# Performance work log

Measured on AMD Instinct MI355X. Metric: run time of the kernel, lower is better.

## Reference

```python
import jax, jax.numpy as jnp
import numpy as np

D_MODEL = 1024
D_MEM = 256


def setup_inputs() -> dict:
    key = jax.random.key(0)
    ks = jax.random.split(key, 12)
    b, s = 4, 2048
    sc_d = 1.0 / np.sqrt(D_MODEL)
    sc_m = 1.0 / np.sqrt(D_MEM)
    return {
        "x": jax.random.normal(ks[0], (b, s, D_MODEL), dtype=jnp.float32),
        "state": jnp.zeros((b, D_MEM, D_MEM), dtype=jnp.float32),
        "Wk": jax.random.normal(ks[1], (D_MODEL, D_MEM), dtype=jnp.float32) * sc_d,
        "bk": jnp.zeros((D_MEM,), dtype=jnp.float32),
        "Wv": jax.random.normal(ks[2], (D_MODEL, D_MEM), dtype=jnp.float32) * sc_d,
        "bv": jnp.zeros((D_MEM,), dtype=jnp.float32),
        "Wq": jax.random.normal(ks[3], (D_MODEL, D_MEM), dtype=jnp.float32) * sc_d,
        "bq": jnp.zeros((D_MEM,), dtype=jnp.float32),
        "Wo": jax.random.normal(ks[4], (D_MEM, D_MODEL), dtype=jnp.float32) * sc_m,
        "bo": jnp.zeros((D_MODEL,), dtype=jnp.float32),
        "Wg": jax.random.normal(ks[5], (D_MODEL, 1), dtype=jnp.float32) * sc_d,
        "bg": jnp.zeros((1,), dtype=jnp.float32),
        "decay": jnp.float32(0.95),
    }


def reference(x, state, Wk, bk, Wv, bv, Wq, bq, Wo, bo, Wg, bg, decay):
    # projections: [b, s, d_mem]
    k = x @ Wk + bk
    v = x @ Wv + bv
    q = x @ Wq + bq
    surprise = jax.nn.sigmoid(x @ Wg + bg)  # [b, s, 1]

    # time-major for scan: [s, b, ...]
    kT = jnp.swapaxes(k, 0, 1)
    vT = jnp.swapaxes(v, 0, 1)
    qT = jnp.swapaxes(q, 0, 1)
    sT = jnp.swapaxes(surprise, 0, 1)  # [s, b, 1]

    def step(S, inp):
        k_t, v_t, q_t, s_t = inp  # [b,dm],[b,dm],[b,dm],[b,1]
        # read: q_t (row) @ S  -> [b, dm]
        mem_out = jnp.einsum('bd,bde->be', q_t, S)
        # write: decayed rank-1 outer-product update, gated by surprise
        assoc = jnp.einsum('bd,be->bde', v_t, k_t)  # v k^T
        S_new = decay * S + s_t[:, :, None] * assoc
        return S_new, mem_out

    final_state, outs = jax.lax.scan(step, state, (kT, vT, qT, sT))
    outputs = jnp.swapaxes(outs, 0, 1)  # [b, s, dm]
    y = outputs @ Wo + bo  # [b, s, d_model]
    return y, final_state
```

## Files before the change

### kernel.cpp

```cpp
#include <hip/hip_runtime.h>
#include <math.h>


using bf16x8 = __attribute__((ext_vector_type(8))) short;
using f32x4  = __attribute__((ext_vector_type(4))) float;
using u16x4  = __attribute__((ext_vector_type(4))) unsigned short;
using u16x8  = __attribute__((ext_vector_type(8))) unsigned short;

__device__ inline unsigned short f2bf(float f) {
  unsigned int u = __float_as_uint(f);
  u = (u + 0x7FFF + ((u >> 16) & 1)) >> 16;
  return (unsigned short)u;
}
__device__ inline float bf2f(unsigned short u) {
  return __uint_as_float(((unsigned int)u) << 16);
}

#define GLD_LDS(gsrc, ldst) \
  __builtin_amdgcn_global_load_lds( \
      (const __attribute__((address_space(1))) unsigned int*)(gsrc), \
      (__attribute__((address_space(3))) unsigned int*)(ldst), 16, 0, 0)

struct MP {
  const unsigned short* A; long long a_bs; int lda;
  const unsigned short* B; long long b_bs; int ldb;
  int K, grid_n;
  unsigned short* Cb; long long c_bs; int ldc;
};

__global__ __launch_bounds__(256)
void gemm_ut(MP p) {
  __shared__ unsigned short As[128 * 64];
  __shared__ unsigned short Bs[128 * 64];
  const int tid = threadIdx.x;
  const int bid = blockIdx.x;
  const int bn = bid % p.grid_n, bm = bid / p.grid_n;
  const int m0 = bm * 128, n0 = bn * 128;
  const long long z = blockIdx.z;
  const int lane = tid & 63, wv = tid >> 6;
  const int wr = wv >> 1, wc = wv & 1;
  const int srow = tid >> 3, scol = (tid & 7) * 8;

  f32x4 acc[4][4] = {};

  const unsigned short* Abase = p.A + z * p.a_bs + (long long)m0 * p.lda;
  const unsigned short* Bbase = p.B + z * p.b_bs + (long long)n0 * p.ldb;

  for (int k0 = 0; k0 < p.K; k0 += 64) {
    if (k0) __syncthreads();
#pragma unroll
    for (int i = 0; i < 4; i++) {
      int row = i * 32 + srow;
      GLD_LDS(Abase + (long long)row * p.lda + k0 + scol, &As[row * 64 + scol]);
    }
#pragma unroll
    for (int i = 0; i < 4; i++) {
      int row = i * 32 + srow;
      GLD_LDS(Bbase + (long long)row * p.ldb + k0 + scol, &Bs[row * 64 + scol]);
    }
    __syncthreads();
#pragma unroll
    for (int kk = 0; kk < 2; kk++) {
      bf16x8 af[4], bfr[4];
      const int kb = kk * 32 + 8 * (lane >> 4);
#pragma unroll
      for (int m = 0; m < 4; m++)
        af[m] = *(const bf16x8*)&As[(wr * 64 + m * 16 + (lane & 15)) * 64 + kb];
#pragma unroll
      for (int n = 0; n < 4; n++)
        bfr[n] = *(const bf16x8*)&Bs[(wc * 64 + n * 16 + (lane & 15)) * 64 + kb];
#pragma unroll
      for (int m = 0; m < 4; m++)
#pragma unroll
        for (int n = 0; n < 4; n++)
          acc[m][n] = __builtin_amdgcn_mfma_f32_16x16x32_bf16(af[m], bfr[n], acc[m][n], 0, 0, 0);
    }
  }

  const int crow0 = m0 + wr * 64, ccol0 = n0 + wc * 64;
#pragma unroll
  for (int m = 0; m < 4; m++) {
#pragma unroll
    for (int n = 0; n < 4; n++) {
      int col = ccol0 + n * 16 + (lane & 15);
#pragma unroll
      for (int q = 0; q < 4; q++) {
        int row = crow0 + m * 16 + (lane >> 4) * 4 + q;
        p.Cb[z * p.c_bs + (long long)row * p.ldc + col] = f2bf(acc[m][n][q]);
      }
    }
  }
}

__global__ __launch_bounds__(256)
void proj_kernel(const unsigned short* __restrict__ x16, const unsigned short* __restrict__ w16,
                 const float* __restrict__ bk, const float* __restrict__ bv,
                 const float* __restrict__ bq, const float* __restrict__ gate,
                 const float* __restrict__ decay_ptr,
                 unsigned short* __restrict__ o_v, unsigned short* __restrict__ o_qd,
                 unsigned short* __restrict__ o_kT, unsigned short* __restrict__ o_vTw) {
  __shared__ unsigned short As[64 * 64];
  __shared__ unsigned short Bs[128 * 64];
  __shared__ float warr[64];
  const int tid = threadIdx.x;
  const int bid = (blockIdx.x & 7) * (gridDim.x >> 3) + (blockIdx.x >> 3);
  const int bn = bid % 6, bm = bid / 6;
  const int m0 = bm * 64, n0 = bn * 128;
  const int lane = tid & 63, wv = tid >> 6;
  const int srow = tid >> 3, scol = (tid & 7) * 8;

  f32x4 acc[4][2] = {};
  const unsigned short* Abase = x16 + (long long)m0 * 1024;
  const unsigned short* Bbase = w16 + (long long)n0 * 1024;

  for (int k0 = 0; k0 < 1024; k0 += 64) {
    if (k0) __syncthreads();
#pragma unroll
    for (int i = 0; i < 2; i++) {
      int row = i * 32 + srow;
      GLD_LDS(Abase + (long long)row * 1024 + k0 + scol, &As[row * 64 + scol]);
    }
#pragma unroll
    for (int i = 0; i < 4; i++) {
      int row = i * 32 + srow;
      GLD_LDS(Bbase + (long long)row * 1024 + k0 + scol, &Bs[row * 64 + scol]);
    }
    __syncthreads();
#pragma unroll
    for (int kk = 0; kk < 2; kk++) {
      const int kb = kk * 32 + 8 * (lane >> 4);
      bf16x8 af[4], bfr[2];
#pragma unroll
      for (int m = 0; m < 4; m++)
        af[m] = *(const bf16x8*)&As[(m * 16 + (lane & 15)) * 64 + kb];
#pragma unroll
      for (int n = 0; n < 2; n++)
        bfr[n] = *(const bf16x8*)&Bs[(wv * 32 + n * 16 + (lane & 15)) * 64 + kb];
#pragma unroll
      for (int m = 0; m < 4; m++)
#pragma unroll
        for (int n = 0; n < 2; n++)
          acc[m][n] = __builtin_amdgcn_mfma_f32_16x16x32_bf16(af[m], bfr[n], acc[m][n], 0, 0, 0);
    }
  }

  const float log2d = log2f(decay_ptr[0]);
  const int sel = bn >> 1;
  const int half = bn & 1;
  const int z = bm >> 1, jbase = (bm & 1) * 64;

  if (sel < 2) {
    __syncthreads();
    if (sel == 1 && tid < 64)
      warr[tid] = gate[z * 128 + jbase + tid] * exp2f((float)(127 - (jbase + tid)) * log2d);
  }

#pragma unroll
  for (int m = 0; m < 4; m++) {
#pragma unroll
    for (int n = 0; n < 2; n++) {
      int cl = wv * 32 + n * 16 + (lane & 15);
      int r0 = m * 16 + (lane >> 4) * 4;
      float bias = (sel == 0) ? bk[half * 128 + cl]
                 : (sel == 1) ? bv[half * 128 + cl]
                 : bq[half * 128 + cl];
      if (sel < 2) {
        u16x4 pk;
#pragma unroll
        for (int q = 0; q < 4; q++) {
          float v = acc[m][n][q] + bias;
          pk[q] = f2bf(v);
          if (sel == 1)
            o_v[((long long)m0 + r0 + q) * 256 + half * 128 + cl] = pk[q];
        }
        int byteoff = (cl * 128 + r0 * 2) ^ ((cl & 7) << 4);
        *(u16x4*)((char*)Bs + byteoff) = pk;
      } else {
#pragma unroll
        for (int q = 0; q < 4; q++) {
          long long row = m0 + r0 + q;
          float v = acc[m][n][q] + bias;
          o_qd[row * 256 + half * 128 + cl] =
              f2bf(v * exp2f((float)(jbase + r0 + q) * log2d));
        }
      }
    }
  }

  if (sel < 2) {
    __syncthreads();
    unsigned short* dst = (sel == 0 ? o_kT : o_vTw) + (long long)z * 32768;
#pragma unroll
    for (int pp = 0; pp < 4; pp++) {
      int idx = pp * 256 + tid;
      int c = idx >> 3;
      int j0 = (idx & 7) * 8;
      u16x8 o = *(const u16x8*)((char*)Bs + ((c * 128 + j0 * 2) ^ ((c & 7) << 4)));
      if (sel == 1) {
#pragma unroll
        for (int t = 0; t < 8; t++) o[t] = f2bf(bf2f(o[t]) * warr[j0 + t]);
      }
      *(u16x8*)&dst[(long long)(half * 128 + c) * 128 + jbase + j0] = o;
    }
  }
}

__global__ __launch_bounds__(256)
void y64_kernel(const unsigned short* __restrict__ mo16, const unsigned short* __restrict__ wot16,
                const float* __restrict__ bo, float* __restrict__ out_y) {
  __shared__ unsigned short As[64 * 64];
  __shared__ unsigned short Bs[128 * 64];
  const int tid = threadIdx.x;
  const int bid = (blockIdx.x & 7) * (gridDim.x >> 3) + (blockIdx.x >> 3);
  const int bn = bid & 7, bm = bid >> 3;
  const int m0 = bm * 64, n0 = bn * 128;
  const int lane = tid & 63, wv = tid >> 6;
  const int srow = tid >> 3, scol = (tid & 7) * 8;

  f32x4 acc[4][2] = {};
  const unsigned short* Abase = mo16 + (long long)m0 * 256;
  const unsigned short* Bbase = wot16 + (long long)n0 * 256;

  for (int k0 = 0; k0 < 256; k0 += 64) {
    if (k0) __syncthreads();
#pragma unroll
    for (int i = 0; i < 2; i++) {
      int row = i * 32 + srow;
      GLD_LDS(Abase + (long long)row * 256 + k0 + scol, &As[row * 64 + scol]);
    }
#pragma unroll
    for (int i = 0; i < 4; i++) {
      int row = i * 32 + srow;
      GLD_LDS(Bbase + (long long)row * 256 + k0 + scol, &Bs[row * 64 + scol]);
    }
    __syncthreads();
#pragma unroll
    for (int kk = 0; kk < 2; kk++) {
      const int kb = kk * 32 + 8 * (lane >> 4);
      bf16x8 af[4], bfr[2];
#pragma unroll
      for (int m = 0; m < 4; m++)
        af[m] = *(const bf16x8*)&As[(m * 16 + (lane & 15)) * 64 + kb];
#pragma unroll
      for (int n = 0; n < 2; n++)
        bfr[n] = *(const bf16x8*)&Bs[(wv * 32 + n * 16 + (lane & 15)) * 64 + kb];
#pragma unroll
      for (int m = 0; m < 4; m++)
#pragma unroll
        for (int n = 0; n < 2; n++)
          acc[m][n] = __builtin_amdgcn_mfma_f32_16x16x32_bf16(af[m], bfr[n], acc[m][n], 0, 0, 0);
    }
  }

#pragma unroll
  for (int m = 0; m < 4; m++) {
#pragma unroll
    for (int n = 0; n < 2; n++) {
      int col = n0 + wv * 32 + n * 16 + (lane & 15);
      float b = bo[col];
#pragma unroll
      for (int q = 0; q < 4; q++) {
        int row = m0 + m * 16 + (lane >> 4) * 4 + q;
        out_y[(long long)row * 1024 + col] = acc[m][n][q] + b;
      }
    }
  }
}

__global__ __launch_bounds__(512)
void chunk_attn(const unsigned short* __restrict__ qd16, const unsigned short* __restrict__ v16,
                const unsigned short* __restrict__ kT16, const unsigned short* __restrict__ T16,
                unsigned short* __restrict__ mo16, const float* __restrict__ gbuf,
                const float* __restrict__ decay_ptr) {
  __shared__ unsigned short As[64 * 64];
  __shared__ unsigned short Bs[2 * 128 * 64];
  __shared__ unsigned short Al[64 * 128];
  const int tid = threadIdx.x, lane = tid & 63, wv = tid >> 6;
  const int wr = wv >> 2, wc = wv & 3;
  const int nh = blockIdx.x, rh = blockIdx.y, z = blockIdx.z;
  const int roff = rh * 64;
  const int srow = tid >> 3, scol = (tid & 7) * 8;
  const float log2d = log2f(decay_ptr[0]);

  const unsigned short* qz = qd16 + (long long)z * 32768 + (long long)roff * 256;
  const unsigned short* vz = v16 + (long long)z * 32768;
  const unsigned short* Tz = T16 + (long long)z * 65536 + (long long)nh * 128 * 256;
  const unsigned short* kz = kT16 + (long long)z * 32768 + (long long)nh * 128 * 128;

  f32x4 acc1[2][2] = {};
  f32x4 acc2[2][2] = {};

  for (int k0 = 0; k0 < 256; k0 += 64) {
    if (k0) __syncthreads();
    GLD_LDS(qz + (long long)srow * 256 + k0 + scol, &As[srow * 64 + scol]);
#pragma unroll
    for (int i = 0; i < 2; i++) {
      int row = i * 64 + srow;
      GLD_LDS(vz + (long long)row * 256 + k0 + scol, &Bs[row * 64 + scol]);
      GLD_LDS(Tz + (long long)row * 256 + k0 + scol, &Bs[8192 + row * 64 + scol]);
    }
    __syncthreads();
#pragma unroll
    for (int kk = 0; kk < 2; kk++) {
      const int kb = kk * 32 + 8 * (lane >> 4);
      bf16x8 af[2], bv[2], bt[2];
#pragma unroll
      for (int m = 0; m < 2; m++)
        af[m] = *(const bf16x8*)&As[(wr * 32 + m * 16 + (lane & 15)) * 64 + kb];
#pragma unroll
      for (int n = 0; n < 2; n++) {
        bv[n] = *(const bf16x8*)&Bs[(wc * 32 + n * 16 + (lane & 15)) * 64 + kb];
        bt[n] = *(const bf16x8*)&Bs[8192 + (wc * 32 + n * 16 + (lane & 15)) * 64 + kb];
      }
#pragma unroll
      for (int m = 0; m < 2; m++)
#pragma unroll
        for (int n = 0; n < 2; n++) {
          acc1[m][n] = __builtin_amdgcn_mfma_f32_16x16x32_bf16(af[m], bv[n], acc1[m][n], 0, 0, 0);
          acc2[m][n] = __builtin_amdgcn_mfma_f32_16x16x32_bf16(af[m], bt[n], acc2[m][n], 0, 0, 0);
        }
    }
  }

#pragma unroll
  for (int n = 0; n < 2; n++) {
    int col = wc * 32 + n * 16 + (lane & 15);
    float gsc = gbuf[z * 128 + col] * exp2f(-(float)(col + 1) * log2d);
#pragma unroll
    for (int m = 0; m < 2; m++) {
#pragma unroll
      for (int q = 0; q < 4; q++) {
        int r = wr * 32 + m * 16 + (lane >> 4) * 4 + q;
        float v = (col < roff + r) ? acc1[m][n][q] * gsc : 0.f;
        int byteoff = (r * 256 + col * 2) ^ ((r & 7) << 4);
        *(unsigned short*)((char*)Al + byteoff) = f2bf(v);
      }
    }
  }
  __syncthreads();

  for (int k0 = 0; k0 < 128; k0 += 64) {
    if (k0) __syncthreads();
#pragma unroll
    for (int i = 0; i < 2; i++) {
      int row = i * 64 + srow;
      GLD_LDS(kz + (long long)row * 128 + k0 + scol, &Bs[row * 64 + scol]);
    }
    __syncthreads();
#pragma unroll
    for (int kk = 0; kk < 2; kk++) {
      const int kbb = k0 + kk * 32 + 8 * (lane >> 4);
      bf16x8 af[2], bk_[2];
#pragma unroll
      for (int m = 0; m < 2; m++) {
        int r = wr * 32 + m * 16 + (lane & 15);
        af[m] = *(const bf16x8*)((char*)Al + ((r * 256 + kbb * 2) ^ ((r & 7) << 4)));
      }
#pragma unroll
      for (int n = 0; n < 2; n++)
        bk_[n] = *(const bf16x8*)&Bs[(wc * 32 + n * 16 + (lane & 15)) * 64 + kk * 32 + 8 * (lane >> 4)];
#pragma unroll
      for (int m = 0; m < 2; m++)
#pragma unroll
        for (int n = 0; n < 2; n++)
          acc2[m][n] = __builtin_amdgcn_mfma_f32_16x16x32_bf16(af[m], bk_[n], acc2[m][n], 0, 0, 0);
    }
  }

#pragma unroll
  for (int m = 0; m < 2; m++) {
#pragma unroll
    for (int n = 0; n < 2; n++) {
      int col = nh * 128 + wc * 32 + n * 16 + (lane & 15);
#pragma unroll
      for (int q = 0; q < 4; q++) {
        int row = roff + wr * 32 + m * 16 + (lane >> 4) * 4 + q;
        mo16[((long long)z * 128 + row) * 256 + col] = f2bf(acc2[m][n][q]);
      }
    }
  }
}

__global__ __launch_bounds__(256)
void prep_kernel(const float* __restrict__ x, const float* __restrict__ Wg,
                 const float* __restrict__ bg, unsigned short* __restrict__ x16,
                 float* __restrict__ g,
                 const float* __restrict__ Wk, const float* __restrict__ Wv,
                 const float* __restrict__ Wq, unsigned short* __restrict__ w16,
                 const float* __restrict__ Wo, unsigned short* __restrict__ wot16) {
  __shared__ float tile[64][65];
  const int bx = blockIdx.x;
  const int tid = threadIdx.x;
  if (bx < 2048) {
    const int wave = tid >> 6, lane = tid & 63;
    const long long row = (long long)bx * 4 + wave;
    const float* xr = x + row * 1024 + lane * 16;
    const float* wr = Wg + lane * 16;
    float s = 0.f;
    u16x8 o0, o1;
#pragma unroll
    for (int qq = 0; qq < 2; qq++) {
      float4 a = *(const float4*)(xr + qq * 4);
      float4 w = *(const float4*)(wr + qq * 4);
      s = fmaf(a.x, w.x, s); s = fmaf(a.y, w.y, s);
      s = fmaf(a.z, w.z, s); s = fmaf(a.w, w.w, s);
      o0[qq * 4 + 0] = f2bf(a.x); o0[qq * 4 + 1] = f2bf(a.y);
      o0[qq * 4 + 2] = f2bf(a.z); o0[qq * 4 + 3] = f2bf(a.w);
    }
#pragma unroll
    for (int qq = 0; qq < 2; qq++) {
      float4 a = *(const float4*)(xr + 8 + qq * 4);
      float4 w = *(const float4*)(wr + 8 + qq * 4);
      s = fmaf(a.x, w.x, s); s = fmaf(a.y, w.y, s);
      s = fmaf(a.z, w.z, s); s = fmaf(a.w, w.w, s);
      o1[qq * 4 + 0] = f2bf(a.x); o1[qq * 4 + 1] = f2bf(a.y);
      o1[qq * 4 + 2] = f2bf(a.z); o1[qq * 4 + 3] = f2bf(a.w);
    }
    *(u16x8*)(x16 + row * 1024 + lane * 16) = o0;
    *(u16x8*)(x16 + row * 1024 + lane * 16 + 8) = o1;
#pragma unroll
    for (int off = 32; off; off >>= 1) s += __shfl_xor(s, off, 64);
    if (lane == 0) g[row] = 1.f / (1.f + expf(-(s + bg[0])));
    return;
  }
  int t = bx - 2048;
  const float* S; unsigned short* dst;
  int srcCols, dstLd, k0, n0g, n0;
  if (t < 192) {
    k0 = (t % 16) * 64; n0g = (t / 16) * 64;
    int sel = n0g >> 8; n0 = n0g - (sel << 8);
    S = sel == 0 ? Wk : sel == 1 ? Wv : Wq;
    srcCols = 256; dst = w16; dstLd = 1024;
  } else {
    t -= 192;
    k0 = (t % 4) * 64; n0g = (t / 4) * 64; n0 = n0g;
    S = Wo; srcCols = 1024; dst = wot16; dstLd = 256;
  }
  const int rr = tid >> 4, c4 = (tid & 15) * 4;
#pragma unroll
  for (int pp = 0; pp < 4; pp++) {
    int r = pp * 16 + rr;
    float4 v = *(const float4*)&S[(long long)(k0 + r) * srcCols + n0 + c4];
    tile[r][c4 + 0] = v.x; tile[r][c4 + 1] = v.y; tile[r][c4 + 2] = v.z; tile[r][c4 + 3] = v.w;
  }
  __syncthreads();
  const int rn = tid >> 3, ck0 = (tid & 7) * 8;
#pragma unroll
  for (int pp = 0; pp < 2; pp++) {
    int n = pp * 32 + rn;
    u16x8 o;
#pragma unroll
    for (int j = 0; j < 8; j++) o[j] = f2bf(tile[ck0 + j][n]);
    *(u16x8*)&dst[(long long)(n0g + n) * dstLd + k0 + ck0] = o;
  }
}

__global__ __launch_bounds__(256)
void scan_kernel(const unsigned short* __restrict__ Ut16, const float* __restrict__ state_in,
                 unsigned short* __restrict__ T16, float* __restrict__ final_out,
                 const float* __restrict__ decay_ptr) {
  int t = blockIdx.x * 256 + threadIdx.x;
  int b = t >> 16, pidx = t & 65535;
  int e = pidx >> 8, d = pidx & 255;
  float dC = exp2f(128.f * log2f(decay_ptr[0]));
  float cur = state_in[(long long)b * 65536 + d * 256 + e];
#pragma unroll
  for (int c = 0; c < 16; c++) {
    long long off = ((long long)(b * 16 + c)) * 65536 + pidx;
    T16[off] = f2bf(cur);
    cur = fmaf(dC, cur, bf2f(Ut16[off]));
  }
  final_out[(long long)b * 65536 + d * 256 + e] = cur;
}

extern "C" void kernel_launch(void* const* d_in, const int* in_sizes, int n_in,
                              void* d_out, int out_size, void* d_ws, size_t ws_size,
                              hipStream_t stream) {
  const float* x     = (const float*)d_in[0];
  const float* state = (const float*)d_in[1];
  const float* Wk = (const float*)d_in[2];  const float* bk = (const float*)d_in[3];
  const float* Wv = (const float*)d_in[4];  const float* bv = (const float*)d_in[5];
  const float* Wq = (const float*)d_in[6];  const float* bq = (const float*)d_in[7];
  const float* Wo = (const float*)d_in[8];  const float* bo = (const float*)d_in[9];
  const float* Wg = (const float*)d_in[10]; const float* bg = (const float*)d_in[11];
  const float* decay = (const float*)d_in[12];

  float* out_y = (float*)d_out;
  float* out_S = out_y + 8388608;

  float* ws = (float*)d_ws;
  unsigned short* x16   = (unsigned short*)(ws);
  unsigned short* v16   = (unsigned short*)(ws + 4194304);
  unsigned short* qd16  = (unsigned short*)(ws + 5242880);
  unsigned short* w16   = (unsigned short*)(ws + 6291456);
  unsigned short* wot16 = (unsigned short*)(ws + 6684672);
  float*          gbuf  = ws + 6815744;
  unsigned short* kT16  = (unsigned short*)(ws + 6823936);
  unsigned short* vTw16 = (unsigned short*)(ws + 7872512);
  unsigned short* Ut16  = (unsigned short*)(ws + 8921088);
  unsigned short* T16   = (unsigned short*)(ws + 11018240);
  unsigned short* mo16  = (unsigned short*)(ws + 13115392);

  prep_kernel<<<2304, 256, 0, stream>>>(x, Wg, bg, x16, gbuf, Wk, Wv, Wq, w16, Wo, wot16);

  proj_kernel<<<768, 256, 0, stream>>>(x16, w16, bk, bv, bq, gbuf, decay,
                                       v16, qd16, kT16, vTw16);

  {
    MP p{};
    p.A = kT16;  p.a_bs = 32768; p.lda = 128;
    p.B = vTw16; p.b_bs = 32768; p.ldb = 128;
    p.K = 128; p.grid_n = 2;
    p.Cb = Ut16; p.c_bs = 65536; p.ldc = 256;
    gemm_ut<<<dim3(4, 1, 64), 256, 0, stream>>>(p);
  }

  scan_kernel<<<1024, 256, 0, stream>>>(Ut16, state, T16, out_S, decay);

  chunk_attn<<<dim3(2, 2, 64), 512, 0, stream>>>(qd16, v16, kT16, T16, mo16, gbuf, decay);

  y64_kernel<<<1024, 256, 0, stream>>>(mo16, wot16, bo, out_y);
}
```

Baseline: 80.56 us.

## Move intra-chunk QV scores into mid kernel alongside Ut GEMM, simplify attention

The masked, gated intra-chunk score matrix (q·v with decay and surprise scaling) is now computed by extra blocks in a merged mid_kernel that also produces the chunk Ut products. The attention kernel then only does two plain GEMMs (q·T and A·kT) with 256 threads instead of recomputing scores per column half. The change also doubles the K tile in proj_kernel to 128 to halve barrier count. It removes duplicated score work and puts it off the critical path before the scan, at the cost of an extra workspace buffer round trip and larger LDS use in proj_kernel.

Result: slower. 96.14 us (+19.3%).

```diff
diff --git a/kernel.cpp b/kernel.cpp
--- a/kernel.cpp
+++ b/kernel.cpp
@@ -20,77 +20,6 @@
   __builtin_amdgcn_global_load_lds( \
       (const __attribute__((address_space(1))) unsigned int*)(gsrc), \
       (__attribute__((address_space(3))) unsigned int*)(ldst), 16, 0, 0)
-
-struct MP {
-  const unsigned short* A; long long a_bs; int lda;
-  const unsigned short* B; long long b_bs; int ldb;
-  int K, grid_n;
-  unsigned short* Cb; long long c_bs; int ldc;
-};
-
-__global__ __launch_bounds__(256)
-void gemm_ut(MP p) {
-  __shared__ unsigned short As[128 * 64];
-  __shared__ unsigned short Bs[128 * 64];
-  const int tid = threadIdx.x;
-  const int bid = blockIdx.x;
-  const int bn = bid % p.grid_n, bm = bid / p.grid_n;
-  const int m0 = bm * 128, n0 = bn * 128;
-  const long long z = blockIdx.z;
-  const int lane = tid & 63, wv = tid >> 6;
-  const int wr = wv >> 1, wc = wv & 1;
-  const int srow = tid >> 3, scol = (tid & 7) * 8;
-
-  f32x4 acc[4][4] = {};
-
-  const unsigned short* Abase = p.A + z * p.a_bs + (long long)m0 * p.lda;
-  const unsigned short* Bbase = p.B + z * p.b_bs + (long long)n0 * p.ldb;
-
-  for (int k0 = 0; k0 < p.K; k0 += 64) {
-    if (k0) __syncthreads();
-#pragma unroll
-    for (int i = 0; i < 4; i++) {
-      int row = i * 32 + srow;
-      GLD_LDS(Abase + (long long)row * p.lda + k0 + scol, &As[row * 64 + scol]);
-    }
-#pragma unroll
-    for (int i = 0; i < 4; i++) {
-      int row = i * 32 + srow;
-      GLD_LDS(Bbase + (long long)row * p.ldb + k0 + scol, &Bs[row * 64 + scol]);
-    }
-    __syncthreads();
-#pragma unroll
-    for (int kk = 0; kk < 2; kk++) {
-      bf16x8 af[4], bfr[4];
-      const int kb = kk * 32 + 8 * (lane >> 4);
-#pragma unroll
-      for (int m = 0; m < 4; m++)
-        af[m] = *(const bf16x8*)&As[(wr * 64 + m * 16 + (lane & 15)) * 64 + kb];
-#pragma unroll
-      for (int n = 0; n < 4; n++)
-        bfr[n] = *(const bf16x8*)&Bs[(wc * 64 + n * 16 + (lane & 15)) * 64 + kb];
-#pragma unroll
-      for (int m = 0; m < 4; m++)
-#pragma unroll
-        for (int n = 0; n < 4; n++)
-          acc[m][n] = __builtin_amdgcn_mfma_f32_16x16x32_bf16(af[m], bfr[n], acc[m][n], 0, 0, 0);
-    }
-  }
-
-  const int crow0 = m0 + wr * 64, ccol0 = n0 + wc * 64;
-#pragma unroll
-  for (int m = 0; m < 4; m++) {
-#pragma unroll
-    for (int n = 0; n < 4; n++) {
-      int col = ccol0 + n * 16 + (lane & 15);
-#pragma unroll
-      for (int q = 0; q < 4; q++) {
-        int row = crow0 + m * 16 + (lane >> 4) * 4 + q;
-        p.Cb[z * p.c_bs + (long long)row * p.ldc + col] = f2bf(acc[m][n][q]);
-      }
-    }
-  }
-}
 
 __global__ __launch_bounds__(256)
 void proj_kernel(const unsigned short* __restrict__ x16, const unsigned short* __restrict__ w16,
@@ -99,43 +28,43 @@
                  const float* __restrict__ decay_ptr,
                  unsigned short* __restrict__ o_v, unsigned short* __restrict__ o_qd,
                  unsigned short* __restrict__ o_kT, unsigned short* __restrict__ o_vTw) {
-  __shared__ unsigned short As[64 * 64];
-  __shared__ unsigned short Bs[128 * 64];
+  __shared__ unsigned short As[64 * 128];
+  __shared__ unsigned short Bs[128 * 128];
   __shared__ float warr[64];
   const int tid = threadIdx.x;
   const int bid = (blockIdx.x & 7) * (gridDim.x >> 3) + (blockIdx.x >> 3);
   const int bn = bid % 6, bm = bid / 6;
   const int m0 = bm * 64, n0 = bn * 128;
   const int lane = tid & 63, wv = tid >> 6;
-  const int srow = tid >> 3, scol = (tid & 7) * 8;
+  const int srow = tid >> 4, scol = (tid & 15) * 8;
 
   f32x4 acc[4][2] = {};
   const unsigned short* Abase = x16 + (long long)m0 * 1024;
   const unsigned short* Bbase = w16 + (long long)n0 * 1024;
 
-  for (int k0 = 0; k0 < 1024; k0 += 64) {
+  for (int k0 = 0; k0 < 1024; k0 += 128) {
     if (k0) __syncthreads();
 #pragma unroll
-    for (int i = 0; i < 2; i++) {
-      int row = i * 32 + srow;
-      GLD_LDS(Abase + (long long)row * 1024 + k0 + scol, &As[row * 64 + scol]);
-    }
-#pragma unroll
     for (int i = 0; i < 4; i++) {
-      int row = i * 32 + srow;
-      GLD_LDS(Bbase + (long long)row * 1024 + k0 + scol, &Bs[row * 64 + scol]);
-    }
-    __syncthreads();
-#pragma unroll
-    for (int kk = 0; kk < 2; kk++) {
+      int row = i * 16 + srow;
+      GLD_LDS(Abase + (long long)row * 1024 + k0 + scol, &As[row * 128 + scol]);
+    }
+#pragma unroll
+    for (int i = 0; i < 8; i++) {
+      int row = i * 16 + srow;
+      GLD_LDS(Bbase + (long long)row * 1024 + k0 + scol, &Bs[row * 128 + scol]);
+    }
+    __syncthreads();
+#pragma unroll
+    for (int kk = 0; kk < 4; kk++) {
       const int kb = kk * 32 + 8 * (lane >> 4);
       bf16x8 af[4], bfr[2];
 #pragma unroll
       for (int m = 0; m < 4; m++)
-        af[m] = *(const bf16x8*)&As[(m * 16 + (lane & 15)) * 64 + kb];
+        af[m] = *(const bf16x8*)&As[(m * 16 + (lane & 15)) * 128 + kb];
 #pragma unroll
       for (int n = 0; n < 2; n++)
-        bfr[n] = *(const bf16x8*)&Bs[(wv * 32 + n * 16 + (lane & 15)) * 64 + kb];
+        bfr[n] = *(const bf16x8*)&Bs[(wv * 32 + n * 16 + (lane & 15)) * 128 + kb];
 #pragma unroll
       for (int m = 0; m < 4; m++)
 #pragma unroll
@@ -201,6 +130,205 @@
         for (int t = 0; t < 8; t++) o[t] = f2bf(bf2f(o[t]) * warr[j0 + t]);
       }
       *(u16x8*)&dst[(long long)(half * 128 + c) * 128 + jbase + j0] = o;
+    }
+  }
+}
+
+__global__ __launch_bounds__(256)
+void mid_kernel(const unsigned short* __restrict__ kT16, const unsigned short* __restrict__ vTw16,
+                unsigned short* __restrict__ Ut16,
+                const unsigned short* __restrict__ qd16, const unsigned short* __restrict__ v16,
+                unsigned short* __restrict__ A16, const float* __restrict__ gbuf,
+                const float* __restrict__ decay_ptr) {
+  __shared__ unsigned short As[128 * 64];
+  __shared__ unsigned short Bs[128 * 64];
+  const int tid = threadIdx.x, lane = tid & 63, wv = tid >> 6;
+  const int wr = wv >> 1, wc = wv & 1;
+  const int srow = tid >> 3, scol = (tid & 7) * 8;
+  f32x4 acc[4][4] = {};
+
+  if (blockIdx.x < 256) {
+    const int b = blockIdx.x;
+    const int z = b >> 2, bm = (b >> 1) & 1, bn = b & 1;
+    const unsigned short* Abase = kT16 + (long long)z * 32768 + (long long)(bm * 128) * 128;
+    const unsigned short* Bbase = vTw16 + (long long)z * 32768 + (long long)(bn * 128) * 128;
+    for (int k0 = 0; k0 < 128; k0 += 64) {
+      if (k0) __syncthreads();
+#pragma unroll
+      for (int i = 0; i < 4; i++) {
+        int row = i * 32 + srow;
+        GLD_LDS(Abase + (long long)row * 128 + k0 + scol, &As[row * 64 + scol]);
+        GLD_LDS(Bbase + (long long)row * 128 + k0 + scol, &Bs[row * 64 + scol]);
+      }
+      __syncthreads();
+#pragma unroll
+      for (int kk = 0; kk < 2; kk++) {
+        const int kb = kk * 32 + 8 * (lane >> 4);
+        bf16x8 af[4], bfr[4];
+#pragma unroll
+        for (int m = 0; m < 4; m++)
+          af[m] = *(const bf16x8*)&As[(wr * 64 + m * 16 + (lane & 15)) * 64 + kb];
+#pragma unroll
+        for (int n = 0; n < 4; n++)
+          bfr[n] = *(const bf16x8*)&Bs[(wc * 64 + n * 16 + (lane & 15)) * 64 + kb];
+#pragma unroll
+        for (int m = 0; m < 4; m++)
+#pragma unroll
+          for (int n = 0; n < 4; n++)
+            acc[m][n] = __builtin_amdgcn_mfma_f32_16x16x32_bf16(af[m], bfr[n], acc[m][n], 0, 0, 0);
+      }
+    }
+    unsigned short* out = Ut16 + (long long)z * 65536;
+#pragma unroll
+    for (int m = 0; m < 4; m++) {
+#pragma unroll
+      for (int n = 0; n < 4; n++) {
+        int col = bn * 128 + wc * 64 + n * 16 + (lane & 15);
+#pragma unroll
+        for (int q = 0; q < 4; q++) {
+          int row = bm * 128 + wr * 64 + m * 16 + (lane >> 4) * 4 + q;
+          out[(long long)row * 256 + col] = f2bf(acc[m][n][q]);
+        }
+      }
+    }
+  } else {
+    const int z = blockIdx.x - 256;
+    const unsigned short* Abase = qd16 + (long long)z * 32768;
+    const unsigned short* Bbase = v16 + (long long)z * 32768;
+    for (int k0 = 0; k0 < 256; k0 += 64) {
+      if (k0) __syncthreads();
+#pragma unroll
+      for (int i = 0; i < 4; i++) {
+        int row = i * 32 + srow;
+        GLD_LDS(Abase + (long long)row * 256 + k0 + scol, &As[row * 64 + scol]);
+        GLD_LDS(Bbase + (long long)row * 256 + k0 + scol, &Bs[row * 64 + scol]);
+      }
+      __syncthreads();
+#pragma unroll
+      for (int kk = 0; kk < 2; kk++) {
+        const int kb = kk * 32 + 8 * (lane >> 4);
+        bf16x8 af[4], bfr[4];
+#pragma unroll
+        for (int m = 0; m < 4; m++)
+          af[m] = *(const bf16x8*)&As[(wr * 64 + m * 16 + (lane & 15)) * 64 + kb];
+#pragma unroll
+        for (int n = 0; n < 4; n++)
+          bfr[n] = *(const bf16x8*)&Bs[(wc * 64 + n * 16 + (lane & 15)) * 64 + kb];
+#pragma unroll
+        for (int m = 0; m < 4; m++)
+#pragma unroll
+          for (int n = 0; n < 4; n++)
+            acc[m][n] = __builtin_amdgcn_mfma_f32_16x16x32_bf16(af[m], bfr[n], acc[m][n], 0, 0, 0);
+      }
+    }
+    const float log2d = log2f(decay_ptr[0]);
+    unsigned short* out = A16 + (long long)z * 16384;
+#pragma unroll
+    for (int n = 0; n < 4; n++) {
+      int col = wc * 64 + n * 16 + (lane & 15);
+      float gsc = gbuf[z * 128 + col] * exp2f(-(float)(col + 1) * log2d);
+#pragma unroll
+      for (int m = 0; m < 4; m++) {
+#pragma unroll
+        for (int q = 0; q < 4; q++) {
+          int row = wr * 64 + m * 16 + (lane >> 4) * 4 + q;
+          float v = (col < row) ? acc[m][n][q] * gsc : 0.f;
+          out[(long long)row * 128 + col] = f2bf(v);
+        }
+      }
+    }
+  }
+}
+
+__global__ __launch_bounds__(256)
+void attn2_kernel(const unsigned short* __restrict__ qd16, const unsigned short* __restrict__ A16,
+                  const unsigned short* __restrict__ kT16, const unsigned short* __restrict__ T16,
+                  unsigned short* __restrict__ mo16) {
+  __shared__ unsigned short As[64 * 64];
+  __shared__ unsigned short Bs[128 * 64];
+  const int tid = threadIdx.x, lane = tid & 63, wv = tid >> 6;
+  const int nh = blockIdx.x, rh = blockIdx.y, z = blockIdx.z;
+  const int roff = rh * 64;
+  const int srow = tid >> 3, scol = (tid & 7) * 8;
+
+  f32x4 acc[4][2] = {};
+  const unsigned short* qz = qd16 + (long long)z * 32768 + (long long)roff * 256;
+  const unsigned short* Tz = T16 + (long long)z * 65536 + (long long)nh * 128 * 256;
+  const unsigned short* Az = A16 + (long long)z * 16384 + (long long)roff * 128;
+  const unsigned short* kz = kT16 + (long long)z * 32768 + (long long)nh * 128 * 128;
+
+  for (int k0 = 0; k0 < 256; k0 += 64) {
+    if (k0) __syncthreads();
+#pragma unroll
+    for (int i = 0; i < 2; i++) {
+      int row = i * 32 + srow;
+      GLD_LDS(qz + (long long)row * 256 + k0 + scol, &As[row * 64 + scol]);
+    }
+#pragma unroll
+    for (int i = 0; i < 4; i++) {
+      int row = i * 32 + srow;
+      GLD_LDS(Tz + (long long)row * 256 + k0 + scol, &Bs[row * 64 + scol]);
+    }
+    __syncthreads();
+#pragma unroll
+    for (int kk = 0; kk < 2; kk++) {
+      const int kb = kk * 32 + 8 * (lane >> 4);
+      bf16x8 af[4], bfr[2];
+#pragma unroll
+      for (int m = 0; m < 4; m++)
+        af[m] = *(const bf16x8*)&As[(m * 16 + (lane & 15)) * 64 + kb];
+#pragma unroll
+      for (int n = 0; n < 2; n++)
+        bfr[n] = *(const bf16x8*)&Bs[(wv * 32 + n * 16 + (lane & 15)) * 64 + kb];
+#pragma unroll
+      for (int m = 0; m < 4; m++)
+#pragma unroll
+        for (int n = 0; n < 2; n++)
+          acc[m][n] = __builtin_amdgcn_mfma_f32_16x16x32_bf16(af[m], bfr[n], acc[m][n], 0, 0, 0);
+    }
+  }
+
+  for (int k0 = 0; k0 < 128; k0 += 64) {
+    __syncthreads();
+#pragma unroll
+    for (int i = 0; i < 2; i++) {
+      int row = i * 32 + srow;
+      GLD_LDS(Az + (long long)row * 128 + k0 + scol, &As[row * 64 + scol]);
+    }
+#pragma unroll
+    for (int i = 0; i < 4; i++) {
+      int row = i * 32 + srow;
+      GLD_LDS(kz + (long long)row * 128 + k0 + scol, &Bs[row * 64 + scol]);
+    }
+    __syncthreads();
+#pragma unroll
+    for (int kk = 0; kk < 2; kk++) {
+      const int kb = kk * 32 + 8 * (lane >> 4);
+      bf16x8 af[4], bfr[2];
+#pragma unroll
+      for (int m = 0; m < 4; m++)
+        af[m] = *(const bf16x8*)&As[(m * 16 + (lane & 15)) * 64 + kb];
+#pragma unroll
+      for (int n = 0; n < 2; n++)
+        bfr[n] = *(const bf16x8*)&Bs[(wv * 32 + n * 16 + (lane & 15)) * 64 + kb];
+#pragma unroll
+      for (int m = 0; m < 4; m++)
+#pragma unroll
+        for (int n = 0; n < 2; n++)
+          acc[m][n] = __builtin_amdgcn_mfma_f32_16x16x32_bf16(af[m], bfr[n], acc[m][n], 0, 0, 0);
+    }
+  }
+
+#pragma unroll
+  for (int m = 0; m < 4; m++) {
+#pragma unroll
+    for (int n = 0; n < 2; n++) {
+      int col = nh * 128 + wv * 32 + n * 16 + (lane & 15);
+#pragma unroll
+      for (int q = 0; q < 4; q++) {
+        int row = roff + m * 16 + (lane >> 4) * 4 + q;
+        mo16[((long long)z * 128 + row) * 256 + col] = f2bf(acc[m][n][q]);
+      }
     }
   }
 }
@@ -262,120 +390,6 @@
       for (int q = 0; q < 4; q++) {
         int row = m0 + m * 16 + (lane >> 4) * 4 + q;
         out_y[(long long)row * 1024 + col] = acc[m][n][q] + b;
-      }
-    }
-  }
-}
-
-__global__ __launch_bounds__(512)
-void chunk_attn(const unsigned short* __restrict__ qd16, const unsigned short* __restrict__ v16,
-                const unsigned short* __restrict__ kT16, const unsigned short* __restrict__ T16,
-                unsigned short* __restrict__ mo16, const float* __restrict__ gbuf,
-                const float* __restrict__ decay_ptr) {
-  __shared__ unsigned short As[64 * 64];
-  __shared__ unsigned short Bs[2 * 128 * 64];
-  __shared__ unsigned short Al[64 * 128];
-  const int tid = threadIdx.x, lane = tid & 63, wv = tid >> 6;
-  const int wr = wv >> 2, wc = wv & 3;
-  const int nh = blockIdx.x, rh = blockIdx.y, z = blockIdx.z;
-  const int roff = rh * 64;
-  const int srow = tid >> 3, scol = (tid & 7) * 8;
-  const float log2d = log2f(decay_ptr[0]);
-
-  const unsigned short* qz = qd16 + (long long)z * 32768 + (long long)roff * 256;
-  const unsigned short* vz = v16 + (long long)z * 32768;
-  const unsigned short* Tz = T16 + (long long)z * 65536 + (long long)nh * 128 * 256;
-  const unsigned short* kz = kT16 + (long long)z * 32768 + (long long)nh * 128 * 128;
-
-  f32x4 acc1[2][2] = {};
-  f32x4 acc2[2][2] = {};
-
-  for (int k0 = 0; k0 < 256; k0 += 64) {
-    if (k0) __syncthreads();
-    GLD_LDS(qz + (long long)srow * 256 + k0 + scol, &As[srow * 64 + scol]);
-#pragma unroll
-    for (int i = 0; i < 2; i++) {
-      int row = i * 64 + srow;
-      GLD_LDS(vz + (long long)row * 256 + k0 + scol, &Bs[row * 64 + scol]);
-      GLD_LDS(Tz + (long long)row * 256 + k0 + scol, &Bs[8192 + row * 64 + scol]);
-    }
-    __syncthreads();
-#pragma unroll
-    for (int kk = 0; kk < 2; kk++) {
-      const int kb = kk * 32 + 8 * (lane >> 4);
-      bf16x8 af[2], bv[2], bt[2];
-#pragma unroll
-      for (int m = 0; m < 2; m++)
-        af[m] = *(const bf16x8*)&As[(wr * 32 + m * 16 + (lane & 15)) * 64 + kb];
-#pragma unroll
-      for (int n = 0; n < 2; n++) {
-        bv[n] = *(const bf16x8*)&Bs[(wc * 32 + n * 16 + (lane & 15)) * 64 + kb];
-        bt[n] = *(const bf16x8*)&Bs[8192 + (wc * 32 + n * 16 + (lane & 15)) * 64 + kb];
-      }
-#pragma unroll
-      for (int m = 0; m < 2; m++)
-#pragma unroll
-        for (int n = 0; n < 2; n++) {
-          acc1[m][n] = __builtin_amdgcn_mfma_f32_16x16x32_bf16(af[m], bv[n], acc1[m][n], 0, 0, 0);
-          acc2[m][n] = __builtin_amdgcn_mfma_f32_16x16x32_bf16(af[m], bt[n], acc2[m][n], 0, 0, 0);
-        }
-    }
-  }
-
-#pragma unroll
-  for (int n = 0; n < 2; n++) {
-    int col = wc * 32 + n * 16 + (lane & 15);
-    float gsc = gbuf[z * 128 + col] * exp2f(-(float)(col + 1) * log2d);
-#pragma unroll
-    for (int m = 0; m < 2; m++) {
-#pragma unroll
-      for (int q = 0; q < 4; q++) {
-        int r = wr * 32 + m * 16 + (lane >> 4) * 4 + q;
-        float v = (col < roff + r) ? acc1[m][n][q] * gsc : 0.f;
-        int byteoff = (r * 256 + col * 2) ^ ((r & 7) << 4);
-        *(unsigned short*)((char*)Al + byteoff) = f2bf(v);
-      }
-    }
-  }
-  __syncthreads();
-
-  for (int k0 = 0; k0 < 128; k0 += 64) {
-    if (k0) __syncthreads();
-#pragma unroll
-    for (int i = 0; i < 2; i++) {
-      int row = i * 64 + srow;
-      GLD_LDS(kz + (long long)row * 128 + k0 + scol, &Bs[row * 64 + scol]);
-    }
-    __syncthreads();
-#pragma unroll
-    for (int kk = 0; kk < 2; kk++) {
-      const int kbb = k0 + kk * 32 + 8 * (lane >> 4);
-      bf16x8 af[2], bk_[2];
-#pragma unroll
-      for (int m = 0; m < 2; m++) {
-        int r = wr * 32 + m * 16 + (lane & 15);
-        af[m] = *(const bf16x8*)((char*)Al + ((r * 256 + kbb * 2) ^ ((r & 7) << 4)));
-      }
-#pragma unroll
-      for (int n = 0; n < 2; n++)
-        bk_[n] = *(const bf16x8*)&Bs[(wc * 32 + n * 16 + (lane & 15)) * 64 + kk * 32 + 8 * (lane >> 4)];
-#pragma unroll
-      for (int m = 0; m < 2; m++)
-#pragma unroll
-        for (int n = 0; n < 2; n++)
-          acc2[m][n] = __builtin_amdgcn_mfma_f32_16x16x32_bf16(af[m], bk_[n], acc2[m][n], 0, 0, 0);
-    }
-  }
-
-#pragma unroll
-  for (int m = 0; m < 2; m++) {
-#pragma unroll
-    for (int n = 0; n < 2; n++) {
-      int col = nh * 128 + wc * 32 + n * 16 + (lane & 15);
-#pragma unroll
-      for (int q = 0; q < 4; q++) {
-        int row = roff + wr * 32 + m * 16 + (lane >> 4) * 4 + q;
-        mo16[((long long)z * 128 + row) * 256 + col] = f2bf(acc2[m][n][q]);
       }
     }
   }
@@ -500,24 +514,18 @@
   unsigned short* Ut16  = (unsigned short*)(ws + 8921088);
   unsigned short* T16   = (unsigned short*)(ws + 11018240);
   unsigned short* mo16  = (unsigned short*)(ws + 13115392);
+  unsigned short* A16   = (unsigned short*)(ws + 14163968);
 
   prep_kernel<<<2304, 256, 0, stream>>>(x, Wg, bg, x16, gbuf, Wk, Wv, Wq, w16, Wo, wot16);
 
   proj_kernel<<<768, 256, 0, stream>>>(x16, w16, bk, bv, bq, gbuf, decay,
                                        v16, qd16, kT16, vTw16);
 
-  {
-    MP p{};
-    p.A = kT16;  p.a_bs = 32768; p.lda = 128;
-    p.B = vTw16; p.b_bs = 32768; p.ldb = 128;
-    p.K = 128; p.grid_n = 2;
-    p.Cb = Ut16; p.c_bs = 65536; p.ldc = 256;
-    gemm_ut<<<dim3(4, 1, 64), 256, 0, stream>>>(p);
-  }
+  mid_kernel<<<320, 256, 0, stream>>>(kT16, vTw16, Ut16, qd16, v16, A16, gbuf, decay);
 
   scan_kernel<<<1024, 256, 0, stream>>>(Ut16, state, T16, out_S, decay);
 
-  chunk_attn<<<dim3(2, 2, 64), 512, 0, stream>>>(qd16, v16, kT16, T16, mo16, gbuf, decay);
+  attn2_kernel<<<dim3(2, 2, 64), 256, 0, stream>>>(qd16, A16, kT16, T16, mo16);
 
   y64_kernel<<<1024, 256, 0, stream>>>(mo16, wot16, bo, out_y);
 }
```
